# Kernel optimization log

Measured on AMD Instinct MI355X. Metric: run time of the kernel, lower is better.

The kernel has to match this reference:

```python
import jax, jax.numpy as jnp
import numpy as np

M, K, N = 8000, 120, 8000
CHUNK_ROW, CHUNK_COL = 128, 64
# padded dims per the module's __init__ arithmetic
M_PAD = (CHUNK_ROW - M % CHUNK_ROW) % CHUNK_ROW + M   # 8064
K_PAD = (CHUNK_COL - K % CHUNK_COL) % CHUNK_COL + K   # 128
N_PAD = (CHUNK_ROW - N % CHUNK_ROW) % CHUNK_ROW + N   # 8064


def setup_inputs() -> dict:
    key = jax.random.key(0)
    kA, kB, kb = jax.random.split(key, 3)
    A = jax.random.normal(kA, (M, K), dtype=jnp.float32)
    Bm = jax.random.normal(kB, (K, N), dtype=jnp.float32)
    bias = jax.random.normal(kb, (N,), dtype=jnp.float32)
    return {"A": A, "Bm": Bm, "bias": bias}


def reference(A, Bm, bias):
    # Zero-pad A to [M_PAD, K_PAD] and B to [K_PAD, N_PAD]; the original
    # blocked loop over (chunk_row, chunk_col) tiles with psum accumulation
    # is mathematically a single dense GEMM on the padded operands.
    A_p = jnp.pad(A, ((0, M_PAD - A.shape[0]), (0, K_PAD - A.shape[1])))
    B_p = jnp.pad(Bm, ((0, K_PAD - Bm.shape[0]), (0, N_PAD - Bm.shape[1])))
    gemm = A_p @ B_p                      # [M_PAD, N_PAD]
    nb = bias.shape[0]
    # bias.shape[0] (=N) != padded N -> add to first nb cols then slice
    gemm = gemm.at[:, :nb].add(bias)
    return gemm[:, :nb]                   # [M_PAD, N]
```

## Files before the change

kernel.cpp:

```cpp
#include <hip/hip_runtime.h>
#include <hip/hip_bf16.h>
#include <stdint.h>

#define M_DIM 8000
#define K_DIM 120
#define N_DIM 8000
#define M_PADD 8064
#define N_PADB 8192
#define K_PADD 128

typedef __attribute__((ext_vector_type(8))) __bf16 bf16x8;
typedef __attribute__((ext_vector_type(4))) float f32x4;
typedef __attribute__((ext_vector_type(8))) unsigned short u16x8;

__device__ __forceinline__ unsigned short f2bf(float f) {
  unsigned int u = __builtin_bit_cast(unsigned int, f);
  u += 0x7FFFu + ((u >> 16) & 1u);
  return (unsigned short)(u >> 16);
}

#define CONV_A_BLOCKS 504
#define CONV_B_BLOCKS 512

__global__ __launch_bounds__(256) void conv_ab_kernel(const float* __restrict__ A,
                                                      const float* __restrict__ B,
                                                      unsigned short* __restrict__ Abf,
                                                      unsigned short* __restrict__ Bbf) {
  const int bid = blockIdx.x;
  if (bid < CONV_A_BLOCKS) {
    int t = bid * 256 + threadIdx.x;
    int row = t >> 4;
    int kg  = t & 15;
    u16x8 v = (u16x8)0;
    if (row < M_DIM && kg < 15) {
      const float* src = A + (size_t)row * K_DIM + kg * 8;
      float4 f0 = *(const float4*)(src);
      float4 f1 = *(const float4*)(src + 4);
      v[0] = f2bf(f0.x); v[1] = f2bf(f0.y); v[2] = f2bf(f0.z); v[3] = f2bf(f0.w);
      v[4] = f2bf(f1.x); v[5] = f2bf(f1.y); v[6] = f2bf(f1.z); v[7] = f2bf(f1.w);
    }
    int off = (kg * 16) ^ ((row & 7) << 4);
    *(u16x8*)((char*)Abf + (size_t)row * 256 + off) = v;
  } else {
    int t = (bid - CONV_A_BLOCKS) * 256 + threadIdx.x;
    int kg = t / N_PADB;
    int n  = t % N_PADB;
    u16x8 v = (u16x8)0;
    if (n < N_DIM && kg < 15) {
      const float* src = B + (size_t)(kg * 8) * N_DIM + n;
#pragma unroll
      for (int j = 0; j < 8; ++j) v[j] = f2bf(src[(size_t)j * N_DIM]);
    }
    int off = (kg * 16) ^ ((n & 7) << 4);
    *(u16x8*)((char*)Bbf + (size_t)n * 256 + off) = v;
  }
}

__global__ __launch_bounds__(256, 3) void gemm_bias_kernel(const unsigned short* __restrict__ Abf,
                                                           const unsigned short* __restrict__ Bbf,
                                                           const float* __restrict__ bias,
                                                           float* __restrict__ out) {
  __shared__ __align__(16) char smem[49152];
  const int bn = blockIdx.x;
  const int bm = blockIdx.y;
  const int tid  = threadIdx.x;
  const int lane = tid & 63;
  const int wave = tid >> 6;

  const char* gA = (const char*)Abf + (size_t)bm * 16384;
  const char* gB = (const char*)Bbf + (size_t)bn * 32768;
#pragma unroll
  for (int i = 0; i < 4; ++i) {
    int off = i * 4096 + tid * 16;
    __builtin_amdgcn_global_load_lds(
        (const __attribute__((address_space(1))) void*)(gA + off),
        (__attribute__((address_space(3))) void*)(smem + off), 16, 0, 0);
  }
#pragma unroll
  for (int i = 0; i < 8; ++i) {
    int off = i * 4096 + tid * 16;
    __builtin_amdgcn_global_load_lds(
        (const __attribute__((address_space(1))) void*)(gB + off),
        (__attribute__((address_space(3))) void*)(smem + 16384 + off), 16, 0, 0);
  }
  __syncthreads();

  f32x4 acc[4][2] = {};
  const int l15 = lane & 15;
  const int kq  = lane >> 4;
#pragma unroll
  for (int ks = 0; ks < 4; ++ks) {
    const int kb = (ks * 32 + kq * 8) * 2;
    bf16x8 a[4], b[2];
#pragma unroll
    for (int m = 0; m < 4; ++m) {
      int row = m * 16 + l15;
      a[m] = *(const bf16x8*)(smem + (size_t)row * 256 + (kb ^ ((row & 7) << 4)));
    }
#pragma unroll
    for (int n = 0; n < 2; ++n) {
      int row = wave * 32 + n * 16 + l15;
      b[n] = *(const bf16x8*)(smem + 16384 + (size_t)row * 256 + (kb ^ ((row & 7) << 4)));
    }
#pragma unroll
    for (int m = 0; m < 4; ++m)
#pragma unroll
      for (int n = 0; n < 2; ++n)
        acc[m][n] = __builtin_amdgcn_mfma_f32_16x16x32_bf16(a[m], b[n], acc[m][n], 0, 0, 0);
  }

  float bv[2];
#pragma unroll
  for (int n = 0; n < 2; ++n) {
    int gcol = bn * 128 + wave * 32 + n * 16 + l15;
    bv[n] = (gcol < N_DIM) ? bias[gcol] : 0.f;
  }

  float* tbuf = (float*)smem;
  __syncthreads();
#pragma unroll
  for (int m = 0; m < 4; ++m)
#pragma unroll
    for (int n = 0; n < 2; ++n)
#pragma unroll
      for (int r = 0; r < 4; ++r) {
        int rl = m * 16 + kq * 4 + r;
        int c  = wave * 32 + n * 16 + l15;
        tbuf[rl * 132 + c] = acc[m][n][r] + bv[n];
      }
  __syncthreads();

  const int c = lane & 31;
  const int gcol0 = bn * 128 + c * 4;
  const bool colok = (gcol0 < N_DIM);
#pragma unroll
  for (int j = 0; j < 8; ++j) {
    int row = j * 8 + wave * 2 + (lane >> 5);
    f32x4 v = *(const f32x4*)(tbuf + row * 132 + c * 4);
    if (colok) {
      size_t off = (size_t)(bm * 64 + row) * N_DIM + gcol0;
      __builtin_nontemporal_store(v, (f32x4*)(out + off));
    }
  }
}

__global__ __launch_bounds__(256) void fallback_kernel(const float* __restrict__ A,
                                                       const float* __restrict__ B,
                                                       const float* __restrict__ bias,
                                                       float* __restrict__ out) {
  size_t idx = (size_t)blockIdx.x * 256 + threadIdx.x;
  if (idx >= (size_t)M_PADD * N_DIM) return;
  int col = (int)(idx % N_DIM);
  int row = (int)(idx / N_DIM);
  float s = 0.f;
  if (row < M_DIM) {
    for (int k = 0; k < K_DIM; ++k)
      s += A[(size_t)row * K_DIM + k] * B[(size_t)k * N_DIM + col];
  }
  out[idx] = s + bias[col];
}

extern "C" void kernel_launch(void* const* d_in, const int* in_sizes, int n_in,
                              void* d_out, int out_size, void* d_ws, size_t ws_size,
                              hipStream_t stream) {
  const float* A    = (const float*)d_in[0];
  const float* Bm   = (const float*)d_in[1];
  const float* bias = (const float*)d_in[2];
  float* out = (float*)d_out;

  const size_t abf_elems = (size_t)M_PADD * K_PADD;
  const size_t bbf_elems = (size_t)N_PADB * K_PADD;
  const size_t need = (abf_elems + bbf_elems) * sizeof(unsigned short);
  if (ws_size < need) {
    size_t total = (size_t)M_PADD * N_DIM;
    fallback_kernel<<<dim3((unsigned)((total + 255) / 256)), dim3(256), 0, stream>>>(A, Bm, bias, out);
    return;
  }

  unsigned short* Abf = (unsigned short*)d_ws;
  unsigned short* Bbf = Abf + abf_elems;

  conv_ab_kernel<<<dim3(CONV_A_BLOCKS + CONV_B_BLOCKS), dim3(256), 0, stream>>>(A, Bm, Abf, Bbf);
  gemm_bias_kernel<<<dim3(63, 126), dim3(256), 0, stream>>>(Abf, Bbf, bias, out);
}
```

Measured before the change: 58.09 us.

## Load GEMM operands directly from global memory and drop LDS staging

The GEMM kernel no longer stages the bf16 A and B tiles through shared memory with an XOR swizzle. Each lane now reads its MFMA fragments straight from global memory, relying on the caches. Shared memory is kept only for the epilogue transpose buffer, which removes the staging barrier and lowers LDS use per block. B's padded width also shrinks from 8192 to 8064 rows, trimming the conversion work. The trade-off is that A fragments are loaded redundantly by all four waves through L1/L2 instead of once into LDS, and the occupancy hint on launch bounds is dropped.

```diff
diff --git a/kernel.cpp b/kernel.cpp
--- a/kernel.cpp
+++ b/kernel.cpp
@@ -6,7 +6,7 @@
 #define K_DIM 120
 #define N_DIM 8000
 #define M_PADD 8064
-#define N_PADB 8192
+#define N_PADB 8064
 #define K_PADD 128
 
 typedef __attribute__((ext_vector_type(8))) __bf16 bf16x8;
@@ -20,7 +20,7 @@
 }
 
 #define CONV_A_BLOCKS 504
-#define CONV_B_BLOCKS 512
+#define CONV_B_BLOCKS 504
 
 __global__ __launch_bounds__(256) void conv_ab_kernel(const float* __restrict__ A,
                                                       const float* __restrict__ B,
@@ -39,8 +39,7 @@
       v[0] = f2bf(f0.x); v[1] = f2bf(f0.y); v[2] = f2bf(f0.z); v[3] = f2bf(f0.w);
       v[4] = f2bf(f1.x); v[5] = f2bf(f1.y); v[6] = f2bf(f1.z); v[7] = f2bf(f1.w);
     }
-    int off = (kg * 16) ^ ((row & 7) << 4);
-    *(u16x8*)((char*)Abf + (size_t)row * 256 + off) = v;
+    *(u16x8*)((char*)Abf + (size_t)row * 256 + kg * 16) = v;
   } else {
     int t = (bid - CONV_A_BLOCKS) * 256 + threadIdx.x;
     int kg = t / N_PADB;
@@ -51,57 +50,36 @@
 #pragma unroll
       for (int j = 0; j < 8; ++j) v[j] = f2bf(src[(size_t)j * N_DIM]);
     }
-    int off = (kg * 16) ^ ((n & 7) << 4);
-    *(u16x8*)((char*)Bbf + (size_t)n * 256 + off) = v;
+    *(u16x8*)((char*)Bbf + (size_t)n * 256 + kg * 16) = v;
   }
 }
 
-__global__ __launch_bounds__(256, 3) void gemm_bias_kernel(const unsigned short* __restrict__ Abf,
-                                                           const unsigned short* __restrict__ Bbf,
-                                                           const float* __restrict__ bias,
-                                                           float* __restrict__ out) {
-  __shared__ __align__(16) char smem[49152];
+__global__ __launch_bounds__(256) void gemm_bias_kernel(const unsigned short* __restrict__ Abf,
+                                                        const unsigned short* __restrict__ Bbf,
+                                                        const float* __restrict__ bias,
+                                                        float* __restrict__ out) {
+  __shared__ __align__(16) float tbuf[64 * 132];
   const int bn = blockIdx.x;
   const int bm = blockIdx.y;
   const int tid  = threadIdx.x;
   const int lane = tid & 63;
   const int wave = tid >> 6;
+  const int l15 = lane & 15;
+  const int kq  = lane >> 4;
 
-  const char* gA = (const char*)Abf + (size_t)bm * 16384;
-  const char* gB = (const char*)Bbf + (size_t)bn * 32768;
-#pragma unroll
-  for (int i = 0; i < 4; ++i) {
-    int off = i * 4096 + tid * 16;
-    __builtin_amdgcn_global_load_lds(
-        (const __attribute__((address_space(1))) void*)(gA + off),
-        (__attribute__((address_space(3))) void*)(smem + off), 16, 0, 0);
-  }
-#pragma unroll
-  for (int i = 0; i < 8; ++i) {
-    int off = i * 4096 + tid * 16;
-    __builtin_amdgcn_global_load_lds(
-        (const __attribute__((address_space(1))) void*)(gB + off),
-        (__attribute__((address_space(3))) void*)(smem + 16384 + off), 16, 0, 0);
-  }
-  __syncthreads();
+  const char* ga = (const char*)Abf + (size_t)(bm * 64 + l15) * 256 + kq * 16;
+  const char* gb = (const char*)Bbf + (size_t)(bn * 128 + wave * 32 + l15) * 256 + kq * 16;
 
   f32x4 acc[4][2] = {};
-  const int l15 = lane & 15;
-  const int kq  = lane >> 4;
 #pragma unroll
   for (int ks = 0; ks < 4; ++ks) {
-    const int kb = (ks * 32 + kq * 8) * 2;
     bf16x8 a[4], b[2];
 #pragma unroll
-    for (int m = 0; m < 4; ++m) {
-      int row = m * 16 + l15;
-      a[m] = *(const bf16x8*)(smem + (size_t)row * 256 + (kb ^ ((row & 7) << 4)));
-    }
+    for (int m = 0; m < 4; ++m)
+      a[m] = *(const bf16x8*)(ga + (size_t)m * 16 * 256 + ks * 64);
 #pragma unroll
-    for (int n = 0; n < 2; ++n) {
-      int row = wave * 32 + n * 16 + l15;
-      b[n] = *(const bf16x8*)(smem + 16384 + (size_t)row * 256 + (kb ^ ((row & 7) << 4)));
-    }
+    for (int n = 0; n < 2; ++n)
+      b[n] = *(const bf16x8*)(gb + (size_t)n * 16 * 256 + ks * 64);
 #pragma unroll
     for (int m = 0; m < 4; ++m)
 #pragma unroll
@@ -116,8 +94,6 @@
     bv[n] = (gcol < N_DIM) ? bias[gcol] : 0.f;
   }
 
-  float* tbuf = (float*)smem;
-  __syncthreads();
 #pragma unroll
   for (int m = 0; m < 4; ++m)
 #pragma unroll
```

After: 106.9 us. +84.0%, slower.
